# Performance work log

Hardware: AMD Instinct MI355X
Metric: run time of the kernel (lower is better)

## Reference

```python
import jax, jax.numpy as jnp
import numpy as np

B, S, W = 64, 128, 20
VOCAB, E, H = 256, 64, 256


def setup_inputs() -> dict:
    key = jax.random.key(0)
    ks = jax.random.split(key, 10)
    return {
        "chars": jax.random.randint(ks[0], (B, S, W), 0, VOCAB),
        "emb": jax.random.uniform(ks[1], (VOCAB, E), jnp.float32, -0.32, 0.32),
        "w1": jax.random.normal(ks[2], (H, E, 1), jnp.float32) * 0.1,
        "b1": jax.random.normal(ks[3], (H,), jnp.float32) * 0.1,
        "w3": jax.random.normal(ks[4], (H, E, 3), jnp.float32) * 0.1,
        "b3": jax.random.normal(ks[5], (H,), jnp.float32) * 0.1,
        "w5": jax.random.normal(ks[6], (H, E, 5), jnp.float32) * 0.1,
        "b5": jax.random.normal(ks[7], (H,), jnp.float32) * 0.1,
        "lw": jax.random.normal(ks[8], (H, 3 * H), jnp.float32) * 0.05,
        "lb": jax.random.normal(ks[9], (H,), jnp.float32) * 0.05,
    }


def _conv_relu_maxpool(x, w, b):
    # x: [N, E, W], w: [H, E, k] ('same' padding k//2) -> [N, H]
    k = w.shape[-1]
    pad = k // 2
    y = jax.lax.conv_general_dilated(
        x, w, window_strides=(1,), padding=[(pad, pad)],
        dimension_numbers=("NCH", "OIH", "NCH"))
    y = jax.nn.relu(y + b[None, :, None])
    return jnp.max(y, axis=2)  # global max over char positions


def reference(chars, emb, w1, b1, w3, b3, w5, b5, lw, lb):
    b, s, wlen = chars.shape
    flat = chars.reshape(-1, wlen)                 # [N, W]
    x = emb[flat]                                  # [N, W, E]
    x = jnp.transpose(x, (0, 2, 1))                # [N, E, W]
    outs = jnp.concatenate([
        _conv_relu_maxpool(x, w1, b1),
        _conv_relu_maxpool(x, w3, b3),
        _conv_relu_maxpool(x, w5, b5),
    ], axis=1)                                     # [N, 3H]
    out = outs @ lw.T + lb                         # [N, H]
    return out.reshape(b, s, -1)
```

## Files before the change

kernel.cpp:

```cpp
#include <hip/hip_runtime.h>
#include <hip/hip_bf16.h>

#define WW 20
#define NW 8192
#define VOCAB 256
#define EE 64
#define HH 256
#define K3 768
#define UNIT4 2560

typedef short bf16x8 __attribute__((ext_vector_type(8)));
typedef float f32x4  __attribute__((ext_vector_type(4)));

__device__ __forceinline__ ushort f2bs(float x) {
    __hip_bfloat16 h = __float2bfloat16(x);
    union { __hip_bfloat16 h; ushort u; } c; c.h = h; return c.u;
}
__device__ __forceinline__ float blo(unsigned u) {
    union { unsigned i; float f; } c; c.i = u << 16; return c.f;
}
__device__ __forceinline__ float bhi(unsigned u) {
    union { unsigned i; float f; } c; c.i = u & 0xffff0000u; return c.f;
}


__global__ __launch_bounds__(256) void prep(
        const float* __restrict__ w1,
        const float* __restrict__ w3,
        const float* __restrict__ w5,
        const float* __restrict__ lw,
        float* __restrict__ wTp,
        ushort* __restrict__ lwb) {
    const int bid = blockIdx.x;
    if (bid < 640) {
        int idx = bid * 256 + threadIdx.x;
        int e = idx / UNIT4;
        int j = idx - e * UNIT4;
        int h = j / 10;
        int tap = j - h * 10;
        float v = 0.f;
        if (tap == 0)      v = w1[h*EE + e];
        else if (tap <= 3) v = w3[(h*EE + e)*3 + (tap-1)];
        else if (tap <= 8) v = w5[(h*EE + e)*5 + (tap-4)];
        wTp[idx] = v;
    } else {
        int i = ((bid - 640) * 256 + threadIdx.x) * 4;
        float4 v = *(const float4*)(lw + i);
        ushort4 o4;
        o4.x = f2bs(v.x); o4.y = f2bs(v.y); o4.z = f2bs(v.z); o4.w = f2bs(v.w);
        *(ushort4*)(lwb + i) = o4;
    }
}

__global__ __launch_bounds__(256) void build_tables(
        const float* __restrict__ emb,
        const float* __restrict__ wTp,
        ushort* __restrict__ P4) {
    __shared__ float emb_s[4][EE];
    const int v0 = blockIdx.x * 4;
    const int j  = blockIdx.y * 256 + threadIdx.x;
    const int t  = threadIdx.x;
    emb_s[t >> 6][t & 63] = emb[v0*EE + t];
    __syncthreads();

    float a0 = 0.f, a1 = 0.f, a2 = 0.f, a3 = 0.f;
    const float* wp = wTp + j;
    #pragma unroll 8
    for (int e = 0; e < EE; ++e) {
        float w = wp[e * UNIT4];
        a0 += emb_s[0][e] * w; a1 += emb_s[1][e] * w;
        a2 += emb_s[2][e] * w; a3 += emb_s[3][e] * w;
    }
    P4[(size_t)(v0+0)*UNIT4 + j] = f2bs(a0);
    P4[(size_t)(v0+1)*UNIT4 + j] = f2bs(a1);
    P4[(size_t)(v0+2)*UNIT4 + j] = f2bs(a2);
    P4[(size_t)(v0+3)*UNIT4 + j] = f2bs(a3);
}

__global__ __launch_bounds__(256) void conv_pool(
        const int* __restrict__ chars,
        const ushort* __restrict__ P4,
        const float* __restrict__ b1,
        const float* __restrict__ b3,
        const float* __restrict__ b5,
        ushort* __restrict__ outs) {
    const int tid  = threadIdx.x;
    const int wave = tid >> 6, lane = tid & 63;
    const int n    = blockIdx.x;
    const int h    = wave * 64 + lane;
    const int hb   = h * 20;

    int cv = chars[n * WW + (lane < WW ? lane : WW - 1)];
    int c[WW];
    #pragma unroll
    for (int j = 0; j < WW; ++j) c[j] = __builtin_amdgcn_readlane(cv, j);

    float acc3[3], acc5[5], m1, m3, m5;
    acc3[0] = 0.f; acc5[0] = 0.f; acc5[1] = 0.f;
    m1 = -1e30f; m3 = -1e30f; m5 = -1e30f;

    uint4 q[2]; unsigned t8[2];
    {
        const char* p = (const char*)P4 + (size_t)c[0] * 5120;
        q[0]  = *(const uint4*)(p + hb);
        t8[0] = *(const unsigned*)(p + hb + 16);
    }

    #pragma unroll
    for (int j = 0; j < WW; ++j) {
        const int cur = j & 1, nxt = cur ^ 1;
        if (j + 1 < WW) {
            const char* p = (const char*)P4 + (size_t)c[j+1] * 5120;
            q[nxt]  = *(const uint4*)(p + hb);
            t8[nxt] = *(const unsigned*)(p + hb + 16);
        }
        uint4 qq = q[cur];
        float t0 = blo(qq.x), t1 = bhi(qq.x), t2 = blo(qq.y), t3 = bhi(qq.y);
        float t4 = blo(qq.z), t5 = bhi(qq.z), t6 = blo(qq.w), t7 = bhi(qq.w);
        float t8v = blo(t8[cur]);

        m1 = fmaxf(m1, t0);
        if (j + 1 < WW) acc3[(j+1)%3] = t1;
        acc3[j%3] += t2;
        if (j >= 1) { acc3[(j-1)%3] += t3;
                      m3 = fmaxf(m3, acc3[(j-1)%3]); }
        if (j + 2 < WW) acc5[(j+2)%5] = t4;
        if (j + 1 < WW) acc5[(j+1)%5] += t5;
        acc5[j%5] += t6;
        if (j >= 1) acc5[(j-1)%5] += t7;
        if (j >= 2) { acc5[(j-2)%5] += t8v;
                      m5 = fmaxf(m5, acc5[(j-2)%5]); }
    }
    m3 = fmaxf(m3, acc3[(WW-1)%3]);
    m5 = fmaxf(m5, acc5[(WW-2)%5]);
    m5 = fmaxf(m5, acc5[(WW-1)%5]);

    float v1 = fmaxf(m1 + b1[h], 0.f);
    float v3 = fmaxf(m3 + b3[h], 0.f);
    float v5 = fmaxf(m5 + b5[h], 0.f);
    ushort* op = outs + (size_t)n * K3 + h;
    op[0*HH] = f2bs(v1);
    op[1*HH] = f2bs(v3);
    op[2*HH] = f2bs(v5);
}

__global__ __launch_bounds__(64) void gemm_out(
        const ushort* __restrict__ outs,
        const ushort* __restrict__ lwb,
        const float* __restrict__ lb,
        float* __restrict__ out) {
    const int lane = threadIdx.x;
    const int m0 = blockIdx.x * 16;
    const int n0 = blockIdx.y * 32;
    const int mrow = lane & 15, quad = lane >> 4;

    f32x4 acc0 = (f32x4){0,0,0,0}, acc1 = (f32x4){0,0,0,0};
    const ushort* ap = outs + (size_t)(m0 + mrow) * K3 + quad * 8;
    const ushort* bp = lwb  + (size_t)(n0 + mrow) * K3 + quad * 8;

    bf16x8 a  = *(const bf16x8*)ap;
    bf16x8 b0 = *(const bf16x8*)bp;
    bf16x8 b1 = *(const bf16x8*)(bp + 16*K3);

    #pragma unroll
    for (int it = 0; it < K3/32; ++it) {
        const int kn = (it + 1 < K3/32) ? (it + 1) * 32 : 0;
        bf16x8 an  = *(const bf16x8*)(ap + kn);
        bf16x8 b0n = *(const bf16x8*)(bp + kn);
        bf16x8 b1n = *(const bf16x8*)(bp + 16*K3 + kn);
        acc0 = __builtin_amdgcn_mfma_f32_16x16x32_bf16(a, b0, acc0, 0, 0, 0);
        acc1 = __builtin_amdgcn_mfma_f32_16x16x32_bf16(a, b1, acc1, 0, 0, 0);
        a = an; b0 = b0n; b1 = b1n;
    }

    #pragma unroll
    for (int nn = 0; nn < 2; ++nn) {
        const f32x4 acc = nn ? acc1 : acc0;
        int ncol = n0 + nn*16 + mrow;
        float lbv = lb[ncol];
        #pragma unroll
        for (int r = 0; r < 4; ++r)
            out[(size_t)(m0 + quad*4 + r)*HH + ncol] = acc[r] + lbv;
    }
}

extern "C" void kernel_launch(void* const* d_in, const int* in_sizes, int n_in,
                              void* d_out, int out_size, void* d_ws, size_t ws_size,
                              hipStream_t stream) {
    const int*   chars = (const int*)d_in[0];
    const float* emb   = (const float*)d_in[1];
    const float* w1    = (const float*)d_in[2];
    const float* b1    = (const float*)d_in[3];
    const float* w3    = (const float*)d_in[4];
    const float* b3    = (const float*)d_in[5];
    const float* w5    = (const float*)d_in[6];
    const float* b5    = (const float*)d_in[7];
    const float* lw    = (const float*)d_in[8];
    const float* lb    = (const float*)d_in[9];

    ushort* P4   = (ushort*)d_ws;
    float*  wTp  = (float*)(P4 + VOCAB * UNIT4);
    ushort* outs = (ushort*)(wTp + EE * UNIT4);
    ushort* lwb  = outs + (size_t)NW * K3;

    prep<<<832, 256, 0, stream>>>(w1, w3, w5, lw, wTp, lwb);
    build_tables<<<dim3(VOCAB/4, 10), 256, 0, stream>>>(emb, wTp, P4);
    conv_pool<<<NW, 256, 0, stream>>>(chars, P4, b1, b3, b5, outs);
    gemm_out<<<dim3(NW/16, HH/32), 64, 0, stream>>>(outs, lwb, lb, (float*)d_out);
}
```

Measured before the change: 160.5 us.

## Stage per-slice projection table in LDS and tile conv over word groups

The precomputed vocab×tap table is repacked into 8-channel slices of 9 taps, dropping the zero padding from 10 to 9 entries per channel. Each conv block loads one slice of the table for the whole vocabulary (36KB) plus 128 words of chars into shared memory, then does its gathers from LDS instead of global memory/L2. The output GEMM also doubles its M tile to 32 rows per wave so each B fragment is reused across two MFMAs. The cost is more LDS per block and 2-way-strided LDS reads that may cause bank conflicts; output writes become strided 8-wide stores.

Result: faster. 134.4 us (-16.2%).

```diff
diff --git a/kernel.cpp b/kernel.cpp
--- a/kernel.cpp
+++ b/kernel.cpp
@@ -7,7 +7,7 @@
 #define EE 64
 #define HH 256
 #define K3 768
-#define UNIT4 2560
+#define UNIT 2304
 
 typedef short bf16x8 __attribute__((ext_vector_type(8)));
 typedef float f32x4  __attribute__((ext_vector_type(4)));
@@ -21,6 +21,9 @@
 }
 __device__ __forceinline__ float bhi(unsigned u) {
     union { unsigned i; float f; } c; c.i = u & 0xffff0000u; return c.f;
+}
+__device__ __forceinline__ float bs2f(ushort u) {
+    union { unsigned i; float f; } c; c.i = ((unsigned)u) << 16; return c.f;
 }
 
 
@@ -32,19 +35,21 @@
         float* __restrict__ wTp,
         ushort* __restrict__ lwb) {
     const int bid = blockIdx.x;
-    if (bid < 640) {
+    if (bid < 576) {
         int idx = bid * 256 + threadIdx.x;
-        int e = idx / UNIT4;
-        int j = idx - e * UNIT4;
-        int h = j / 10;
-        int tap = j - h * 10;
-        float v = 0.f;
+        int e = idx / UNIT;
+        int j = idx - e * UNIT;
+        int s = j / 72, r = j - s * 72;
+        int tap, h;
+        if (r < 64) { tap = r & 7; h = s*8 + (r >> 3); }
+        else        { tap = 8;     h = s*8 + (r - 64); }
+        float v;
         if (tap == 0)      v = w1[h*EE + e];
         else if (tap <= 3) v = w3[(h*EE + e)*3 + (tap-1)];
-        else if (tap <= 8) v = w5[(h*EE + e)*5 + (tap-4)];
+        else               v = w5[(h*EE + e)*5 + (tap-4)];
         wTp[idx] = v;
     } else {
-        int i = ((bid - 640) * 256 + threadIdx.x) * 4;
+        int i = ((bid - 576) * 256 + threadIdx.x) * 4;
         float4 v = *(const float4*)(lw + i);
         ushort4 o4;
         o4.x = f2bs(v.x); o4.y = f2bs(v.y); o4.z = f2bs(v.z); o4.w = f2bs(v.w);
@@ -55,7 +60,7 @@
 __global__ __launch_bounds__(256) void build_tables(
         const float* __restrict__ emb,
         const float* __restrict__ wTp,
-        ushort* __restrict__ P4) {
+        ushort* __restrict__ P5) {
     __shared__ float emb_s[4][EE];
     const int v0 = blockIdx.x * 4;
     const int j  = blockIdx.y * 256 + threadIdx.x;
@@ -67,81 +72,98 @@
     const float* wp = wTp + j;
     #pragma unroll 8
     for (int e = 0; e < EE; ++e) {
-        float w = wp[e * UNIT4];
+        float w = wp[e * UNIT];
         a0 += emb_s[0][e] * w; a1 += emb_s[1][e] * w;
         a2 += emb_s[2][e] * w; a3 += emb_s[3][e] * w;
     }
-    P4[(size_t)(v0+0)*UNIT4 + j] = f2bs(a0);
-    P4[(size_t)(v0+1)*UNIT4 + j] = f2bs(a1);
-    P4[(size_t)(v0+2)*UNIT4 + j] = f2bs(a2);
-    P4[(size_t)(v0+3)*UNIT4 + j] = f2bs(a3);
+    P5[(size_t)(v0+0)*UNIT + j] = f2bs(a0);
+    P5[(size_t)(v0+1)*UNIT + j] = f2bs(a1);
+    P5[(size_t)(v0+2)*UNIT + j] = f2bs(a2);
+    P5[(size_t)(v0+3)*UNIT + j] = f2bs(a3);
 }
 
 __global__ __launch_bounds__(256) void conv_pool(
         const int* __restrict__ chars,
-        const ushort* __restrict__ P4,
+        const ushort* __restrict__ P5,
         const float* __restrict__ b1,
         const float* __restrict__ b3,
         const float* __restrict__ b5,
         ushort* __restrict__ outs) {
-    const int tid  = threadIdx.x;
-    const int wave = tid >> 6, lane = tid & 63;
-    const int n    = blockIdx.x;
-    const int h    = wave * 64 + lane;
-    const int hb   = h * 20;
-
-    int cv = chars[n * WW + (lane < WW ? lane : WW - 1)];
-    int c[WW];
-    #pragma unroll
-    for (int j = 0; j < WW; ++j) c[j] = __builtin_amdgcn_readlane(cv, j);
-
-    float acc3[3], acc5[5], m1, m3, m5;
-    acc3[0] = 0.f; acc5[0] = 0.f; acc5[1] = 0.f;
-    m1 = -1e30f; m3 = -1e30f; m5 = -1e30f;
-
-    uint4 q[2]; unsigned t8[2];
+    __shared__ uint4 tileq[2304];
+    __shared__ int   chs[128*WW];
+    const int t = threadIdx.x;
+    const int g = blockIdx.x;
+    const int s = blockIdx.y;
+
     {
-        const char* p = (const char*)P4 + (size_t)c[0] * 5120;
-        q[0]  = *(const uint4*)(p + hb);
-        t8[0] = *(const unsigned*)(p + hb + 16);
-    }
-
-    #pragma unroll
-    for (int j = 0; j < WW; ++j) {
-        const int cur = j & 1, nxt = cur ^ 1;
-        if (j + 1 < WW) {
-            const char* p = (const char*)P4 + (size_t)c[j+1] * 5120;
-            q[nxt]  = *(const uint4*)(p + hb);
-            t8[nxt] = *(const unsigned*)(p + hb + 16);
+        const char* src = (const char*)P5 + (size_t)s * 144;
+        char* dst = (char*)tileq;
+        #pragma unroll
+        for (int i = 0; i < 9; ++i) {
+            int c = i*256 + t;
+            int v = c / 9, k = c - 9*v;
+            *(uint4*)(dst + v*144 + k*16) =
+                *(const uint4*)(src + (size_t)v*4608 + k*16);
         }
-        uint4 qq = q[cur];
-        float t0 = blo(qq.x), t1 = bhi(qq.x), t2 = blo(qq.y), t3 = bhi(qq.y);
-        float t4 = blo(qq.z), t5 = bhi(qq.z), t6 = blo(qq.w), t7 = bhi(qq.w);
-        float t8v = blo(t8[cur]);
-
-        m1 = fmaxf(m1, t0);
-        if (j + 1 < WW) acc3[(j+1)%3] = t1;
-        acc3[j%3] += t2;
-        if (j >= 1) { acc3[(j-1)%3] += t3;
-                      m3 = fmaxf(m3, acc3[(j-1)%3]); }
-        if (j + 2 < WW) acc5[(j+2)%5] = t4;
-        if (j + 1 < WW) acc5[(j+1)%5] += t5;
-        acc5[j%5] += t6;
-        if (j >= 1) acc5[(j-1)%5] += t7;
-        if (j >= 2) { acc5[(j-2)%5] += t8v;
-                      m5 = fmaxf(m5, acc5[(j-2)%5]); }
-    }
-    m3 = fmaxf(m3, acc3[(WW-1)%3]);
-    m5 = fmaxf(m5, acc5[(WW-2)%5]);
-    m5 = fmaxf(m5, acc5[(WW-1)%5]);
-
-    float v1 = fmaxf(m1 + b1[h], 0.f);
-    float v3 = fmaxf(m3 + b3[h], 0.f);
-    float v5 = fmaxf(m5 + b5[h], 0.f);
-    ushort* op = outs + (size_t)n * K3 + h;
-    op[0*HH] = f2bs(v1);
-    op[1*HH] = f2bs(v3);
-    op[2*HH] = f2bs(v5);
+        const int* cg = chars + g * 128 * WW;
+        #pragma unroll
+        for (int i = 0; i < 10; ++i) chs[i*256 + t] = cg[i*256 + t];
+    }
+    __syncthreads();
+
+    const int hl  = t & 7;
+    const int wl0 = t >> 3;
+    const char* tile = (const char*)tileq;
+
+    for (int cc = 0; cc < 4; ++cc) {
+        const int wl = cc*32 + wl0;
+        const int n  = g*128 + wl;
+        const int* cw = &chs[wl*WW];
+
+        float acc3[3], acc5[5];
+        float m1 = -1e30f, m3 = -1e30f, m5 = -1e30f;
+        acc3[0] = 0.f; acc5[0] = 0.f; acc5[1] = 0.f;
+
+        int c_cur = cw[0];
+        uint4 q[2]; ushort t8[2];
+        q[0]  = *(const uint4*)(tile + c_cur*144 + hl*16);
+        t8[0] = *(const ushort*)(tile + c_cur*144 + 128 + hl*2);
+
+        #pragma unroll
+        for (int j = 0; j < WW; ++j) {
+            const int cur = j & 1, nxt = cur ^ 1;
+            if (j + 1 < WW) {
+                int c_n = cw[j+1];
+                q[nxt]  = *(const uint4*)(tile + c_n*144 + hl*16);
+                t8[nxt] = *(const ushort*)(tile + c_n*144 + 128 + hl*2);
+            }
+            uint4 qq = q[cur];
+            float t0 = blo(qq.x), t1 = bhi(qq.x), t2 = blo(qq.y), t3 = bhi(qq.y);
+            float t4 = blo(qq.z), t5 = bhi(qq.z), t6 = blo(qq.w), t7 = bhi(qq.w);
+            float t8v = bs2f(t8[cur]);
+
+            m1 = fmaxf(m1, t0);
+            if (j + 1 < WW) acc3[(j+1)%3] = t1;
+            acc3[j%3] += t2;
+            if (j >= 1) { acc3[(j-1)%3] += t3;
+                          m3 = fmaxf(m3, acc3[(j-1)%3]); }
+            if (j + 2 < WW) acc5[(j+2)%5] = t4;
+            if (j + 1 < WW) acc5[(j+1)%5] += t5;
+            acc5[j%5] += t6;
+            if (j >= 1) acc5[(j-1)%5] += t7;
+            if (j >= 2) { acc5[(j-2)%5] += t8v;
+                          m5 = fmaxf(m5, acc5[(j-2)%5]); }
+        }
+        m3 = fmaxf(m3, acc3[(WW-1)%3]);
+        m5 = fmaxf(m5, acc5[(WW-2)%5]);
+        m5 = fmaxf(m5, acc5[(WW-1)%5]);
+
+        const int h = s*8 + hl;
+        ushort* op = outs + (size_t)n * K3 + h;
+        op[0*HH] = f2bs(fmaxf(m1 + b1[h], 0.f));
+        op[1*HH] = f2bs(fmaxf(m3 + b3[h], 0.f));
+        op[2*HH] = f2bs(fmaxf(m5 + b5[h], 0.f));
+    }
 }
 
 __global__ __launch_bounds__(64) void gemm_out(
@@ -150,37 +172,44 @@
         const float* __restrict__ lb,
         float* __restrict__ out) {
     const int lane = threadIdx.x;
-    const int m0 = blockIdx.x * 16;
+    const int m0 = blockIdx.x * 32;
     const int n0 = blockIdx.y * 32;
     const int mrow = lane & 15, quad = lane >> 4;
 
-    f32x4 acc0 = (f32x4){0,0,0,0}, acc1 = (f32x4){0,0,0,0};
+    f32x4 acc00 = (f32x4){0,0,0,0}, acc01 = (f32x4){0,0,0,0};
+    f32x4 acc10 = (f32x4){0,0,0,0}, acc11 = (f32x4){0,0,0,0};
     const ushort* ap = outs + (size_t)(m0 + mrow) * K3 + quad * 8;
     const ushort* bp = lwb  + (size_t)(n0 + mrow) * K3 + quad * 8;
 
-    bf16x8 a  = *(const bf16x8*)ap;
-    bf16x8 b0 = *(const bf16x8*)bp;
-    bf16x8 b1 = *(const bf16x8*)(bp + 16*K3);
+    bf16x8 a0 = *(const bf16x8*)ap, a1 = *(const bf16x8*)(ap + 16*K3);
+    bf16x8 b0 = *(const bf16x8*)bp, b1 = *(const bf16x8*)(bp + 16*K3);
 
     #pragma unroll
     for (int it = 0; it < K3/32; ++it) {
         const int kn = (it + 1 < K3/32) ? (it + 1) * 32 : 0;
-        bf16x8 an  = *(const bf16x8*)(ap + kn);
+        bf16x8 a0n = *(const bf16x8*)(ap + kn);
+        bf16x8 a1n = *(const bf16x8*)(ap + 16*K3 + kn);
         bf16x8 b0n = *(const bf16x8*)(bp + kn);
         bf16x8 b1n = *(const bf16x8*)(bp + 16*K3 + kn);
-        acc0 = __builtin_amdgcn_mfma_f32_16x16x32_bf16(a, b0, acc0, 0, 0, 0);
-        acc1 = __builtin_amdgcn_mfma_f32_16x16x32_bf16(a, b1, acc1, 0, 0, 0);
-        a = an; b0 = b0n; b1 = b1n;
+        acc00 = __builtin_amdgcn_mfma_f32_16x16x32_bf16(a0, b0, acc00, 0, 0, 0);
+        acc01 = __builtin_amdgcn_mfma_f32_16x16x32_bf16(a0, b1, acc01, 0, 0, 0);
+        acc10 = __builtin_amdgcn_mfma_f32_16x16x32_bf16(a1, b0, acc10, 0, 0, 0);
+        acc11 = __builtin_amdgcn_mfma_f32_16x16x32_bf16(a1, b1, acc11, 0, 0, 0);
+        a0 = a0n; a1 = a1n; b0 = b0n; b1 = b1n;
     }
 
     #pragma unroll
-    for (int nn = 0; nn < 2; ++nn) {
-        const f32x4 acc = nn ? acc1 : acc0;
-        int ncol = n0 + nn*16 + mrow;
-        float lbv = lb[ncol];
-        #pragma unroll
-        for (int r = 0; r < 4; ++r)
-            out[(size_t)(m0 + quad*4 + r)*HH + ncol] = acc[r] + lbv;
+    for (int i = 0; i < 2; ++i) {
+        #pragma unroll
+        for (int jn = 0; jn < 2; ++jn) {
+            const f32x4 acc = (i==0) ? (jn==0 ? acc00 : acc01)
+                                     : (jn==0 ? acc10 : acc11);
+            int ncol = n0 + jn*16 + mrow;
+            float lbv = lb[ncol];
+            #pragma unroll
+            for (int r = 0; r < 4; ++r)
+                out[(size_t)(m0 + i*16 + quad*4 + r)*HH + ncol] = acc[r] + lbv;
+        }
     }
 }
 
@@ -198,13 +227,13 @@
     const float* lw    = (const float*)d_in[8];
     const float* lb    = (const float*)d_in[9];
 
-    ushort* P4   = (ushort*)d_ws;
-    float*  wTp  = (float*)(P4 + VOCAB * UNIT4);
-    ushort* outs = (ushort*)(wTp + EE * UNIT4);
+    ushort* P5   = (ushort*)d_ws;
+    float*  wTp  = (float*)(P5 + VOCAB * UNIT);
+    ushort* outs = (ushort*)(wTp + EE * UNIT);
     ushort* lwb  = outs + (size_t)NW * K3;
 
-    prep<<<832, 256, 0, stream>>>(w1, w3, w5, lw, wTp, lwb);
-    build_tables<<<dim3(VOCAB/4, 10), 256, 0, stream>>>(emb, wTp, P4);
-    conv_pool<<<NW, 256, 0, stream>>>(chars, P4, b1, b3, b5, outs);
-    gemm_out<<<dim3(NW/16, HH/32), 64, 0, stream>>>(outs, lwb, lb, (float*)d_out);
-}
+    prep<<<768, 256, 0, stream>>>(w1, w3, w5, lw, wTp, lwb);
+    build_tables<<<dim3(VOCAB/4, 9), 256, 0, stream>>>(emb, wTp, P5);
+    conv_pool<<<dim3(NW/128, 32), 256, 0, stream>>>(chars, P5, b1, b3, b5, outs);
+    gemm_out<<<dim3(NW/32, HH/32), 64, 0, stream>>>(outs, lwb, lb, (float*)d_out);
+}
```
